# Performance work log

Measured on AMD Instinct MI355X. Metric: run time of the kernel, lower is better.

## Reference

```python
import jax, jax.numpy as jnp
import numpy as np

N = 1024      # n_nodes
F = 64        # n_features
L = 64        # lookback_window (must equal F for U1 @ B to typecheck, as in the torch code)
NDF = 4       # n_data_features
NTF = 8       # n_time_features
FC1 = 1024
FC2 = 512
K = 2         # kernel_size
DIL = (2, 2)  # dilation_list
DELTA = 0.05
EPS = 1e-5


def _ln(x, g, b):
    mu = x.mean(-1, keepdims=True)
    v = ((x - mu) ** 2).mean(-1, keepdims=True)
    return (x - mu) / jnp.sqrt(v + EPS) * g + b


def _mlp2(x, W1, b1, g, bb, W2, b2):
    h = jax.nn.relu(_ln(x @ W1 + b1, g, bb))
    return h @ W2 + b2


def setup_inputs() -> dict:
    ks = jax.random.split(jax.random.key(0), 16)
    def rn(i, shape, s=1.0):
        return jax.random.normal(ks[i], shape, dtype=jnp.float32) * s
    z = lambda *s: jnp.zeros(s, jnp.float32)
    o = lambda *s: jnp.ones(s, jnp.float32)
    return {
        "observation": rn(0, (N, NDF, L)),
        "time_features": rn(1, (L, NTF)),
        "layer_initial": rn(2, (L, N)),
        "sW1": rn(3, (N, 256), N ** -0.5), "sb1": z(256), "s_ln_g": o(256), "s_ln_b": z(256),
        "sW2": rn(4, (256, N * F), 256 ** -0.5), "sb2": z(N * F),
        "tW1": rn(5, (NTF, 256), NTF ** -0.5), "tb1": z(256), "t_ln_g": o(256), "t_ln_b": z(256),
        "tW2": rn(6, (256, N * F), 256 ** -0.5), "tb2": z(N * F),
        "B": o(F, F),
        "fW1": rn(7, (N * NDF, FC1), (N * NDF) ** -0.5), "fb1": z(FC1), "f1g": o(FC1), "f1b": z(FC1),
        "fW2": rn(8, (FC1, FC2), FC1 ** -0.5), "fb2": z(FC2), "f2g": o(FC2), "f2b": z(FC2),
        "fW3": rn(9, (FC2, N * F), FC2 ** -0.5), "fb3": z(N * F),
        "Wf": rn(10, (K, F, F)), "Wb": rn(11, (K, F, F)), "bconv": rn(12, (F,)),
    }


def _forward(observation, time_features, layer_initial, sW1, sb1, s_ln_g, s_ln_b, sW2, sb2,
             tW1, tb1, t_ln_g, t_ln_b, tW2, tb2, B,
             fW1, fb1, f1g, f1b, fW2, fb2, f2g, f2b, fW3, fb3, Wf, Wb, bconv):
    # GraphConstructor node embedding; U[:, :, j] is (N, L)
    emb = _mlp2(layer_initial, sW1, sb1, s_ln_g, s_ln_b, sW2, sb2) \
        + _mlp2(time_features, tW1, tb1, t_ln_g, t_ln_b, tW2, tb2)   # (L, N*F)
    U = emb.reshape(L, N, F).transpose(1, 0, 2)                      # (N, L, F)
    Uf = jnp.moveaxis(U, 2, 0)                                       # (F, N, L) for feature-axis gathers

    def adj(aidx, bidx):
        # batched adjacency: softmax over rows of thresholded U1 B U2^T, then D^-1/2 A D^-1/2
        Ua, Ub = Uf[aidx], Uf[bidx]                                  # (M, N, L)
        S = jax.lax.stop_gradient(jnp.einsum('mnl,lp,mqp->mnq', Ua, B, Ub))  # .detach() in torch
        S = jnp.where(S >= DELTA, S, 0.0)
        A = jax.nn.softmax(S, axis=-1)
        dn = 1.0 / jnp.sqrt(A.sum(-1))                               # degree is diagonal -> sqrtm/inverse = elementwise
        return A * dn[:, :, None] * dn[:, None, :]

    # fully_connected: observation (N, NDF, L) -> X (N, F, L)
    obs = observation.transpose(2, 0, 1).reshape(L, N * NDF)
    h = jax.nn.relu(_ln(obs @ fW1 + fb1, f1g, f1b))
    h = jax.nn.relu(_ln(h @ fW2 + fb2, f2g, f2b))
    X = (h @ fW3 + fb3).reshape(L, N, F).transpose(1, 2, 0)          # (N, F, L)

    gamma = 1
    outs = []
    for d in DIL:
        length = X.shape[-1]
        ts = np.arange(d - 1, length, d)                             # t with (t+1) % d == 0, static
        Z = jnp.zeros((ts.size, N, F), X.dtype)
        for k in range(K):
            tk = ts - k                                              # >= 0 since K <= min(DIL)
            Xk = X[:, :, tk]                                         # (N, F, M)
            A1 = adj((gamma * tk) % L, (gamma * ts) % L)             # pair (idx - k*gamma, idx)
            A2 = adj((gamma * ts) % L, (gamma * tk) % L)             # pair (idx, idx - k*gamma)
            msg = jnp.einsum('mnq,qfm->mnf', A1, Xk) @ Wf[k] \
                + jnp.einsum('mnq,qfm->mnf', A2, Xk) @ Wb[k] + bconv
            Z = Z + jnp.tanh(msg)
        X = jnp.moveaxis(Z, 0, 2)                                    # (N, F, M) becomes next layer input
        outs.append(X[:, :, -1])
        gamma *= d
    return jnp.stack(outs)                                           # (len(DIL), N, F)


def reference(observation, time_features, layer_initial, sW1, sb1, s_ln_g, s_ln_b, sW2, sb2,
              tW1, tb1, t_ln_g, t_ln_b, tW2, tb2, B,
              fW1, fb1, f1g, f1b, fW2, fb2, f2g, f2b, fW3, fb3, Wf, Wb, bconv):
    return _forward(observation, time_features, layer_initial, sW1, sb1, s_ln_g, s_ln_b, sW2, sb2,
                    tW1, tb1, t_ln_g, t_ln_b, tW2, tb2, B,
                    fW1, fb1, f1g, f1b, fW2, fb2, f2g, f2b, fW3, fb3, Wf, Wb, bconv)
```

## Files before the change

### kernel.cpp

```cpp
#include <hip/hip_runtime.h>
#include <cstddef>

#define EPS_C   1e-5f
#define DELTA_C 0.05f

struct Pairs { int a[6]; int b[6]; int t[6]; };


template<int K>
__device__ __forceinline__ void head_body(
    const float* __restrict__ A, const float* __restrict__ W1,
    const float* __restrict__ b1, const float* __restrict__ g,
    const float* __restrict__ bb, float* __restrict__ H,
    float* As, float* rs, float* rs2, int row, int j)
{
  for (int i = j; i < K; i += 256) As[i] = A[row * K + i];
  __syncthreads();

  float a0 = 0.f, a1 = 0.f, a2 = 0.f, a3 = 0.f;
  const float* __restrict__ Wp = W1 + j;
#pragma unroll 2
  for (int c = 0; c < K; c += 8) {
    float w0 = Wp[(size_t)(c + 0) * 256];
    float w1 = Wp[(size_t)(c + 1) * 256];
    float w2 = Wp[(size_t)(c + 2) * 256];
    float w3 = Wp[(size_t)(c + 3) * 256];
    float w4 = Wp[(size_t)(c + 4) * 256];
    float w5 = Wp[(size_t)(c + 5) * 256];
    float w6 = Wp[(size_t)(c + 6) * 256];
    float w7 = Wp[(size_t)(c + 7) * 256];
    a0 += As[c + 0] * w0 + As[c + 4] * w4;
    a1 += As[c + 1] * w1 + As[c + 5] * w5;
    a2 += As[c + 2] * w2 + As[c + 6] * w6;
    a3 += As[c + 3] * w3 + As[c + 7] * w7;
  }
  float acc = ((a0 + a1) + (a2 + a3)) + b1[j];

  rs[j] = acc; rs2[j] = acc * acc;
  __syncthreads();
  for (int st = 128; st > 0; st >>= 1) {
    if (j < st) { rs[j] += rs[j + st]; rs2[j] += rs2[j + st]; }
    __syncthreads();
  }
  float mu  = rs[0] * (1.f / 256.f);
  float var = rs2[0] * (1.f / 256.f) - mu * mu;
  float y = (acc - mu) * rsqrtf(var + EPS_C) * g[j] + bb[j];
  H[row * 256 + j] = fmaxf(y, 0.f);
}

template<int MODE>
__device__ __forceinline__ void skinny_body(
    const float* __restrict__ A, const float* __restrict__ W,
    float* __restrict__ part, int K, int N, int bid, int tid,
    float (*ARs)[64])
{
  int jblocks = N >> 8;
  int jb = bid % jblocks;
  int kc = bid / jblocks;
  int k0 = kc << 6;
  {
    int c = tid >> 6, i = tid & 63;
    int k = k0 + i;
    float v;
    if (MODE == 0) v = A[c * K + k];
    else { int n = k >> 2, df = k & 3; v = A[n * 256 + df * 64 + 60 + c]; }
    ARs[c][i] = v;
  }
  __syncthreads();
  int j = (jb << 8) + tid;
  float acc0 = 0.f, acc1 = 0.f, acc2 = 0.f, acc3 = 0.f;
#pragma unroll
  for (int kk = 0; kk < 64; kk += 16) {
    float w[16];
#pragma unroll
    for (int u = 0; u < 16; ++u) w[u] = W[(size_t)(k0 + kk + u) * N + j];
#pragma unroll
    for (int u = 0; u < 16; ++u) {
      acc0 += ARs[0][kk + u] * w[u];
      acc1 += ARs[1][kk + u] * w[u];
      acc2 += ARs[2][kk + u] * w[u];
      acc3 += ARs[3][kk + u] * w[u];
    }
  }
  part[(size_t)(kc * 4 + 0) * N + j] = acc0;
  part[(size_t)(kc * 4 + 1) * N + j] = acc1;
  part[(size_t)(kc * 4 + 2) * N + j] = acc2;
  part[(size_t)(kc * 4 + 3) * N + j] = acc3;
}

template<int N_, int PARTS>
__device__ __forceinline__ void red_body(
    const float* __restrict__ part, const float* __restrict__ bias,
    const float* __restrict__ g, const float* __restrict__ bb,
    float* __restrict__ out, int c, int tid, float* rs, float* rs2)
{
  constexpr int PER = N_ >> 8;
  float x[PER];
  float s = 0.f, s2 = 0.f;
#pragma unroll
  for (int i = 0; i < PER; ++i) {
    int j = (i << 8) + tid;
    float v = bias[j];
#pragma unroll 8
    for (int p = 0; p < PARTS; ++p) v += part[(size_t)(p * 4 + c) * N_ + j];
    x[i] = v; s += v; s2 += v * v;
  }
  rs[tid] = s; rs2[tid] = s2;
  __syncthreads();
  for (int st = 128; st > 0; st >>= 1) {
    if (tid < st) { rs[tid] += rs[tid + st]; rs2[tid] += rs2[tid + st]; }
    __syncthreads();
  }
  float mu  = rs[0] / (float)N_;
  float var = rs2[0] / (float)N_ - mu * mu;
  float inv = rsqrtf(var + EPS_C);
#pragma unroll
  for (int i = 0; i < PER; ++i) {
    int j = (i << 8) + tid;
    out[c * N_ + j] = fmaxf((x[i] - mu) * inv * g[j] + bb[j], 0.f);
  }
}


__global__ __launch_bounds__(256) void k1_heads_skinny(
    const float* __restrict__ layer_initial, const float* __restrict__ sW1,
    const float* __restrict__ sb1, const float* __restrict__ s_g,
    const float* __restrict__ s_b, float* __restrict__ Hs,
    const float* __restrict__ time_features, const float* __restrict__ tW1,
    const float* __restrict__ tb1, const float* __restrict__ t_g,
    const float* __restrict__ t_b, float* __restrict__ Ht,
    const float* __restrict__ observation, const float* __restrict__ fW1,
    float* __restrict__ part1)
{
  __shared__ float As[1024];
  __shared__ float rs[256], rs2[256];
  __shared__ float ARs[4][64];
  int bid = blockIdx.x, j = threadIdx.x;
  if (bid < 64) {
    head_body<1024>(layer_initial, sW1, sb1, s_g, s_b, Hs, As, rs, rs2, bid, j);
  } else if (bid < 128) {
    head_body<8>(time_features, tW1, tb1, t_g, t_b, Ht, As, rs, rs2, bid - 64, j);
  } else {
    skinny_body<1>(observation, fW1, part1, 4096, 1024, bid - 128, j, ARs);
  }
}

__global__ __launch_bounds__(256) void k2_emb_red1(
    const float* __restrict__ Hs, const float* __restrict__ Ht,
    const float* __restrict__ sW2, const float* __restrict__ sb2,
    const float* __restrict__ tW2, const float* __restrict__ tb2,
    float* __restrict__ Vs,
    const float* __restrict__ part1, const float* __restrict__ fb1,
    const float* __restrict__ f1g, const float* __restrict__ f1b,
    float* __restrict__ h1)
{
  __shared__ __align__(16) float HcT[64][68];
  __shared__ __align__(16) float Wc[64][20];
  int tid = threadIdx.x;
  if (blockIdx.x < 256) {
    int n0 = blockIdx.x * 4;
    int lq = tid >> 4, jc = tid & 15;
    int nn = n0 + (jc >> 2), cc = jc & 3;
    int kkw = tid >> 2, nloc = tid & 3;

    float4 hr[4]; float4 wr;
    {
      const float* __restrict__ Hsrc = Hs;
      const float* __restrict__ Wsrc = sW2;
#pragma unroll
      for (int i = 0; i < 4; ++i) {
        int flat = i * 1024 + tid * 4;
        int l = flat >> 6, kk = flat & 63;
        hr[i] = *(const float4*)&Hsrc[l * 256 + kk];
      }
      wr = *(const float4*)&Wsrc[(size_t)kkw * 65536 + (size_t)(n0 + nloc) * 64 + 60];
    }
    float acc0 = 0.f, acc1 = 0.f, acc2 = 0.f, acc3 = 0.f;
    for (int ch = 0; ch < 8; ++ch) {
      __syncthreads();
#pragma unroll
      for (int i = 0; i < 4; ++i) {
        int flat = i * 1024 + tid * 4;
        int l = flat >> 6, kk = flat & 63;
        HcT[kk + 0][l] = hr[i].x;
        HcT[kk + 1][l] = hr[i].y;
        HcT[kk + 2][l] = hr[i].z;
        HcT[kk + 3][l] = hr[i].w;
      }
      *(float4*)&Wc[kkw][nloc * 4] = wr;
      __syncthreads();
      if (ch < 7) {
        int nc2 = ch + 1;
        const float* __restrict__ Hsrc = (nc2 < 4) ? Hs : Ht;
        const float* __restrict__ Wsrc = (nc2 < 4) ? sW2 : tW2;
        int kl = (nc2 & 3) << 6;
#pragma unroll
        for (int i = 0; i < 4; ++i) {
          int flat = i * 1024 + tid * 4;
          int l = flat >> 6, kk = flat & 63;
          hr[i] = *(const float4*)&Hsrc[l * 256 + kl + kk];
        }
        wr = *(const float4*)&Wsrc[(size_t)(kl + kkw) * 65536 + (size_t)(n0 + nloc) * 64 + 60];
      }
#pragma unroll 8
      for (int kk = 0; kk < 64; ++kk) {
        float4 av = *(const float4*)&HcT[kk][lq * 4];
        float w = Wc[kk][jc];
        acc0 += av.x * w; acc1 += av.y * w; acc2 += av.z * w; acc3 += av.w * w;
      }
    }
    int jj = nn * 64 + 60 + cc;
    float bias = sb2[jj] + tb2[jj];
    float4 st = { acc0 + bias, acc1 + bias, acc2 + bias, acc3 + bias };
    *(float4*)&Vs[(size_t)cc * 65536 + (size_t)nn * 64 + lq * 4] = st;
  } else {
    red_body<1024, 64>(part1, fb1, f1g, f1b, h1, blockIdx.x - 256, tid,
                       &HcT[0][0], &HcT[0][0] + 256);
  }
}

__global__ __launch_bounds__(256) void k3_vab_skinny(
    const float* __restrict__ Vs, const float* __restrict__ Bmat,
    float* __restrict__ VaBt, float* __restrict__ VsT,
    const float* __restrict__ h1, const float* __restrict__ fW2,
    float* __restrict__ part2)
{
  __shared__ float Va[64][65], Bs[64][65];
  int tid = threadIdx.x;
  if (blockIdx.x < 64) {
    int c = blockIdx.x >> 4, nb = blockIdx.x & 15;
    int n0 = nb << 6;
    int rg = tid >> 4, cg = tid & 15;
#pragma unroll
    for (int i = 0; i < 4; ++i) {
      int flat = i * 1024 + tid * 4;
      int rr = flat >> 6, cc = flat & 63;
      float4 v = *(const float4*)&Vs[(size_t)c * 65536 + (size_t)(n0 + rr) * 64 + cc];
      Va[rr][cc] = v.x; Va[rr][cc+1] = v.y; Va[rr][cc+2] = v.z; Va[rr][cc+3] = v.w;
      float4 w = *(const float4*)&Bmat[flat];
      Bs[rr][cc] = w.x; Bs[rr][cc+1] = w.y; Bs[rr][cc+2] = w.z; Bs[rr][cc+3] = w.w;
    }
    __syncthreads();
#pragma unroll
    for (int i = 0; i < 4; ++i) {
      int flat = i * 1024 + tid * 4;
      int l = flat >> 6, nn = flat & 63;
      float4 st = { Va[nn][l], Va[nn+1][l], Va[nn+2][l], Va[nn+3][l] };
      *(float4*)&VsT[(size_t)c * 65536 + (size_t)l * 1024 + n0 + nn] = st;
    }
    float acc[4][4];
#pragma unroll
    for (int i = 0; i < 4; ++i)
#pragma unroll
      for (int j = 0; j < 4; ++j) acc[i][j] = 0.f;
#pragma unroll 4
    for (int l = 0; l < 64; ++l) {
      float av[4], bv[4];
#pragma unroll
      for (int i = 0; i < 4; ++i) av[i] = Va[rg * 4 + i][l];
#pragma unroll
      for (int j = 0; j < 4; ++j) bv[j] = Bs[l][cg * 4 + j];
#pragma unroll
      for (int i = 0; i < 4; ++i)
#pragma unroll
        for (int j = 0; j < 4; ++j) acc[i][j] += av[i] * bv[j];
    }
#pragma unroll
    for (int j = 0; j < 4; ++j) {
      float4 st = { acc[0][j], acc[1][j], acc[2][j], acc[3][j] };
      *(float4*)&VaBt[(size_t)c * 65536 + (size_t)(cg * 4 + j) * 1024 + n0 + rg * 4] = st;
    }
  } else {
    skinny_body<0>(h1, fW2, part2, 1024, 512, blockIdx.x - 64, tid,
                   (float(*)[64])&Va[0][0]);
  }
}

__global__ __launch_bounds__(256) void big_w3b(
    const float* __restrict__ part2, const float* __restrict__ fb2,
    const float* __restrict__ f2g, const float* __restrict__ f2b,
    const float* __restrict__ fW3, const float* __restrict__ fb3,
    float* __restrict__ Xr)
{
  int tid = threadIdx.x;
  __shared__ float h2s[2048];
  __shared__ float sm[4][128];
  {
    int c = tid >> 6, lane = tid & 63;
    float v[8]; float s = 0.f, s2 = 0.f;
#pragma unroll
    for (int k = 0; k < 8; ++k) {
      int j = lane + k * 64;
      float x = fb2[j];
#pragma unroll
      for (int p = 0; p < 16; ++p) x += part2[(size_t)(p * 4 + c) * 512 + j];
      v[k] = x; s += x; s2 += x * x;
    }
#pragma unroll
    for (int off = 1; off < 64; off <<= 1) {
      s += __shfl_xor(s, off); s2 += __shfl_xor(s2, off);
    }
    float mu = s * (1.f / 512.f);
    float var = s2 * (1.f / 512.f) - mu * mu;
    float inv = rsqrtf(var + EPS_C);
#pragma unroll
    for (int k = 0; k < 8; ++k) {
      int j = lane + k * 64;
      h2s[c * 512 + j] = fmaxf((v[k] - mu) * inv * f2g[j] + f2b[j], 0.f);
    }
  }
  __syncthreads();

  int col = tid & 127, ks = tid >> 7;
  int j = blockIdx.x * 128 + col;
  int kbase = ks << 8;
  float acc0 = 0.f, acc1 = 0.f, acc2 = 0.f, acc3 = 0.f;
  for (int k0 = 0; k0 < 256; k0 += 16) {
    float w[16];
#pragma unroll
    for (int u = 0; u < 16; ++u) w[u] = fW3[(size_t)(kbase + k0 + u) * 65536 + j];
#pragma unroll
    for (int u = 0; u < 16; ++u) {
      int k = kbase + k0 + u;
      acc0 += h2s[k]        * w[u];
      acc1 += h2s[512 + k]  * w[u];
      acc2 += h2s[1024 + k] * w[u];
      acc3 += h2s[1536 + k] * w[u];
    }
  }
  if (ks) { sm[0][col] = acc0; sm[1][col] = acc1; sm[2][col] = acc2; sm[3][col] = acc3; }
  __syncthreads();
  if (!ks) {
    float b = fb3[j];
    Xr[j]            = acc0 + sm[0][col] + b;
    Xr[65536 + j]    = acc1 + sm[1][col] + b;
    Xr[131072 + j]   = acc2 + sm[2][col] + b;
    Xr[196608 + j]   = acc3 + sm[3][col] + b;
  }
}

template<int NSPLIT>
__global__ __launch_bounds__(256) void attn_partial(
    const float* __restrict__ VaBt, const float* __restrict__ VsT,
    const float* __restrict__ Xbase, float* __restrict__ Pl,
    float* __restrict__ ml, Pairs pr)
{
  constexpr int TILES = 16 / NSPLIT;
  int pi  = blockIdx.x / (16 * NSPLIT);
  int rem = blockIdx.x % (16 * NSPLIT);
  int nb  = rem / NSPLIT;
  int s   = rem % NSPLIT;
  int n0  = nb << 6;
  int tid = threadIdx.x;
  int rg = tid >> 4, cg = tid & 15;
  int rg4 = rg * 4, cg4 = cg * 4;
  int a = pr.a[pi], b = pr.b[pi], t = pr.t[pi];

  __shared__ __align__(16) float VaT[64][68];
  __shared__ __align__(16) float VbT[64][68];
  __shared__ __align__(16) float Xs[64][68];
  float (*St)[68] = VbT;

#pragma unroll
  for (int i = 0; i < 4; ++i) {
    int flat = i * 1024 + tid * 4;
    int p = flat >> 6, nn = flat & 63;
    float4 v = *(const float4*)&VaBt[(size_t)a * 65536 + (size_t)p * 1024 + n0 + nn];
    *(float4*)&VaT[p][nn] = v;
  }
  float m_run[4], l_run[4];
#pragma unroll
  for (int i = 0; i < 4; ++i) { m_run[i] = -1e30f; l_run[i] = 0.f; }
  float P[4][4];
#pragma unroll
  for (int i = 0; i < 4; ++i)
#pragma unroll
    for (int j = 0; j < 4; ++j) P[i][j] = 0.f;
  __syncthreads();

  for (int ti = 0; ti < TILES; ++ti) {
    int q0 = (s * TILES + ti) << 6;
    if (ti) __syncthreads();
#pragma unroll
    for (int i = 0; i < 4; ++i) {
      int flat = i * 1024 + tid * 4;
      int p = flat >> 6, qq = flat & 63;
      float4 v = *(const float4*)&VsT[(size_t)b * 65536 + (size_t)p * 1024 + q0 + qq];
      *(float4*)&VbT[p][qq] = v;
      float4 x = *(const float4*)&Xbase[(size_t)t * 65536 + (size_t)(q0 + p) * 64 + qq];
      *(float4*)&Xs[p][qq] = x;
    }
    __syncthreads();
    float sa[4][4];
#pragma unroll
    for (int i = 0; i < 4; ++i)
#pragma unroll
      for (int j = 0; j < 4; ++j) sa[i][j] = 0.f;
#pragma unroll 4
    for (int p = 0; p < 64; ++p) {
      float av[4], bv[4];
      *(float4*)av = *(const float4*)&VaT[p][rg4];
      *(float4*)bv = *(const float4*)&VbT[p][cg4];
#pragma unroll
      for (int i = 0; i < 4; ++i)
#pragma unroll
        for (int j = 0; j < 4; ++j) sa[i][j] += av[i] * bv[j];
    }
    float scv[4];
#pragma unroll
    for (int i = 0; i < 4; ++i) {
#pragma unroll
      for (int j = 0; j < 4; ++j) sa[i][j] = (sa[i][j] >= DELTA_C) ? sa[i][j] : 0.f;
      float tm = fmaxf(fmaxf(sa[i][0], sa[i][1]), fmaxf(sa[i][2], sa[i][3]));
      tm = fmaxf(tm, __shfl_xor(tm, 1));
      tm = fmaxf(tm, __shfl_xor(tm, 2));
      tm = fmaxf(tm, __shfl_xor(tm, 4));
      tm = fmaxf(tm, __shfl_xor(tm, 8));
      float mnew = fmaxf(m_run[i], tm);
      float sc = __expf(m_run[i] - mnew);
      float ssum = 0.f;
#pragma unroll
      for (int j = 0; j < 4; ++j) {
        float e = __expf(sa[i][j] - mnew);
        sa[i][j] = e;
        ssum += e;
      }
      ssum += __shfl_xor(ssum, 1);
      ssum += __shfl_xor(ssum, 2);
      ssum += __shfl_xor(ssum, 4);
      ssum += __shfl_xor(ssum, 8);
      l_run[i] = l_run[i] * sc + ssum;
      m_run[i] = mnew;
      scv[i] = sc;
    }
    __syncthreads();
#pragma unroll
    for (int i = 0; i < 4; ++i) {
      float4 e4 = { sa[i][0], sa[i][1], sa[i][2], sa[i][3] };
      *(float4*)&St[rg4 + i][cg4] = e4;
    }
    __syncthreads();
#pragma unroll
    for (int i = 0; i < 4; ++i)
#pragma unroll
      for (int j = 0; j < 4; ++j) P[i][j] *= scv[i];
#pragma unroll 2
    for (int q4 = 0; q4 < 64; q4 += 4) {
      float4 ev[4], xv[4];
#pragma unroll
      for (int i = 0; i < 4; ++i) ev[i] = *(const float4*)&St[rg4 + i][q4];
#pragma unroll
      for (int u = 0; u < 4; ++u) xv[u] = *(const float4*)&Xs[q4 + u][cg4];
#pragma unroll
      for (int i = 0; i < 4; ++i) {
        const float* e = &ev[i].x;
#pragma unroll
        for (int u = 0; u < 4; ++u) {
          const float* x = &xv[u].x;
#pragma unroll
          for (int j = 0; j < 4; ++j) P[i][j] += e[u] * x[j];
        }
      }
    }
  }
  size_t base = (size_t)((pi * 16 + nb) * NSPLIT + s);
  float* pp = Pl + base * 4096;
#pragma unroll
  for (int i = 0; i < 4; ++i) {
    float4 st = { P[i][0], P[i][1], P[i][2], P[i][3] };
    *(float4*)&pp[(size_t)(rg4 + i) * 64 + cg4] = st;
  }
  if ((tid & 15) == 0) {
    float* mlp = ml + base * 128;
#pragma unroll
    for (int i = 0; i < 4; ++i) {
      mlp[rg4 + i]      = m_run[i];
      mlp[64 + rg4 + i] = l_run[i];
    }
  }
}

template<int NS_T>
__global__ __launch_bounds__(256) void merge_partial(
    const float* __restrict__ Pl, const float* __restrict__ ml,
    const float* __restrict__ Wf, const float* __restrict__ Wb,
    float* __restrict__ Gp)
{
  int mm = blockIdx.x / 48;
  int rem = blockIdx.x % 48;
  int nb = rem / 3, inst = rem % 3;
  int n0 = nb << 6;
  int tid = threadIdx.x;
  int rg = tid >> 4, cg = tid & 15;
  int rg4 = rg * 4, cg4 = cg * 4;
  int r = tid >> 2, sub = tid & 3;

  __shared__ __align__(16) float PtT[64][68];
  __shared__ __align__(16) float Wt[64][68];

  size_t base = (size_t)((mm * 3 + inst) * 16 + nb) * NS_T;
  const float* mlp = ml + base * 128;
  float mg = -1e30f;
#pragma unroll
  for (int s2 = 0; s2 < NS_T; ++s2) mg = fmaxf(mg, mlp[s2 * 128 + r]);
  float acc[16];
#pragma unroll
  for (int u = 0; u < 16; ++u) acc[u] = 0.f;
  float lg = 0.f;
#pragma unroll
  for (int s2 = 0; s2 < NS_T; ++s2) {
    float f = __expf(mlp[s2 * 128 + r] - mg);
    lg += f * mlp[s2 * 128 + 64 + r];
    const float4* ps = (const float4*)(Pl + (base + s2) * 4096 + r * 64 + sub * 16);
#pragma unroll
    for (int u = 0; u < 4; ++u) {
      float4 v = ps[u];
      acc[u*4+0] += f * v.x; acc[u*4+1] += f * v.y;
      acc[u*4+2] += f * v.z; acc[u*4+3] += f * v.w;
    }
  }
  float inv = 1.f / lg;
#pragma unroll
  for (int u = 0; u < 16; ++u) PtT[sub * 16 + u][r] = acc[u] * inv;
  for (int i = tid; i < 4096; i += 256) {
    int rr = i >> 6, cc = i & 63;
    float w;
    if (inst == 0)      w = Wf[i] + Wb[i];
    else if (inst == 1) w = Wf[4096 + i];
    else                w = Wb[4096 + i];
    Wt[rr][cc] = w;
  }
  __syncthreads();
  float g2[4][4];
#pragma unroll
  for (int i = 0; i < 4; ++i)
#pragma unroll
    for (int j = 0; j < 4; ++j) g2[i][j] = 0.f;
#pragma unroll 4
  for (int ff = 0; ff < 64; ++ff) {
    float p[4], w[4];
    *(float4*)p = *(const float4*)&PtT[ff][rg4];
    *(float4*)w = *(const float4*)&Wt[ff][cg4];
#pragma unroll
    for (int i = 0; i < 4; ++i)
#pragma unroll
      for (int j = 0; j < 4; ++j) g2[i][j] += p[i] * w[j];
  }
#pragma unroll
  for (int i = 0; i < 4; ++i) {
    float4 st = { g2[i][0], g2[i][1], g2[i][2], g2[i][3] };
    *(float4*)&Gp[(size_t)(mm * 3 + inst) * 65536 + (size_t)(n0 + rg4 + i) * 64 + cg4] = st;
  }
}

__global__ __launch_bounds__(256) void finalize_z(
    const float* __restrict__ Gp, const float* __restrict__ bconv,
    float* __restrict__ dst0, float* __restrict__ dst1, float* __restrict__ extra1)
{
  int mm = blockIdx.x >> 4;
  int nb = blockIdx.x & 15;
  int tid = threadIdx.x;
  size_t tileOff = (size_t)(nb << 6) * 64;
  const float* g0 = Gp + (size_t)(mm * 3 + 0) * 65536 + tileOff;
  const float* g1 = Gp + (size_t)(mm * 3 + 1) * 65536 + tileOff;
  const float* g2 = Gp + (size_t)(mm * 3 + 2) * 65536 + tileOff;
  float* dst = (mm == 0) ? dst0 : dst1;
  for (int i = tid * 4; i < 4096; i += 1024) {
    float4 a = *(const float4*)&g0[i];
    float4 b = *(const float4*)&g1[i];
    float4 c = *(const float4*)&g2[i];
    int col = i & 63;
    float4 z;
    z.x = tanhf(a.x + bconv[col+0]) + tanhf(b.x + c.x + bconv[col+0]);
    z.y = tanhf(a.y + bconv[col+1]) + tanhf(b.y + c.y + bconv[col+1]);
    z.z = tanhf(a.z + bconv[col+2]) + tanhf(b.z + c.z + bconv[col+2]);
    z.w = tanhf(a.w + bconv[col+3]) + tanhf(b.w + c.w + bconv[col+3]);
    *(float4*)&dst[tileOff + i] = z;
    if (mm == 1 && extra1) *(float4*)&extra1[tileOff + i] = z;
  }
}

extern "C" void kernel_launch(void* const* d_in, const int* in_sizes, int n_in,
                              void* d_out, int out_size, void* d_ws, size_t ws_size,
                              hipStream_t stream)
{
  const float* observation   = (const float*)d_in[0];
  const float* time_features = (const float*)d_in[1];
  const float* layer_initial = (const float*)d_in[2];
  const float* sW1   = (const float*)d_in[3];
  const float* sb1   = (const float*)d_in[4];
  const float* s_ln_g = (const float*)d_in[5];
  const float* s_ln_b = (const float*)d_in[6];
  const float* sW2   = (const float*)d_in[7];
  const float* sb2   = (const float*)d_in[8];
  const float* tW1   = (const float*)d_in[9];
  const float* tb1   = (const float*)d_in[10];
  const float* t_ln_g = (const float*)d_in[11];
  const float* t_ln_b = (const float*)d_in[12];
  const float* tW2   = (const float*)d_in[13];
  const float* tb2   = (const float*)d_in[14];
  const float* Bmat  = (const float*)d_in[15];
  const float* fW1   = (const float*)d_in[16];
  const float* fb1   = (const float*)d_in[17];
  const float* f1g   = (const float*)d_in[18];
  const float* f1b   = (const float*)d_in[19];
  const float* fW2   = (const float*)d_in[20];
  const float* fb2   = (const float*)d_in[21];
  const float* f2g   = (const float*)d_in[22];
  const float* f2b   = (const float*)d_in[23];
  const float* fW3   = (const float*)d_in[24];
  const float* fb3   = (const float*)d_in[25];
  const float* Wf    = (const float*)d_in[26];
  const float* Wb    = (const float*)d_in[27];
  const float* bconv = (const float*)d_in[28];
  float* out = (float*)d_out;

  float* ws    = (float*)d_ws;
  float* Hs    = ws;
  float* Ht    = Hs    + 16384;
  float* Vs    = Ht    + 16384;
  float* VsT   = Vs    + 262144;
  float* VaBt  = VsT   + 262144;
  float* part1 = VaBt  + 262144;
  float* part2 = part1 + 262144;
  float* h1    = part2 + 32768;
  float* Xr    = h1    + 4096;
  float* Pl    = Xr    + 262144;
  float* ml    = Pl    + 3145728;
  float* Pl2   = ml    + 98304;
  float* ml2   = Pl2   + 3145728;
  float* Z1    = ml2   + 98304;
  float* Gp    = Z1    + 131072;

  k1_heads_skinny<<<384, 256, 0, stream>>>(
      layer_initial, sW1, sb1, s_ln_g, s_ln_b, Hs,
      time_features, tW1, tb1, t_ln_g, t_ln_b, Ht,
      observation, fW1, part1);
  k2_emb_red1<<<260, 256, 0, stream>>>(
      Hs, Ht, sW2, sb2, tW2, tb2, Vs,
      part1, fb1, f1g, f1b, h1);
  k3_vab_skinny<<<96, 256, 0, stream>>>(Vs, Bmat, VaBt, VsT, h1, fW2, part2);
  big_w3b<<<512, 256, 0, stream>>>(part2, fb2, f2g, f2b, fW3, fb3, Xr);

  Pairs pA;
  pA.a[0]=1; pA.b[0]=1; pA.t[0]=1;
  pA.a[1]=0; pA.b[1]=1; pA.t[1]=0;
  pA.a[2]=1; pA.b[2]=0; pA.t[2]=0;
  pA.a[3]=3; pA.b[3]=3; pA.t[3]=3;
  pA.a[4]=2; pA.b[4]=3; pA.t[4]=2;
  pA.a[5]=3; pA.b[5]=2; pA.t[5]=2;
  attn_partial<8><<<6 * 16 * 8, 256, 0, stream>>>(VaBt, VsT, Xr, Pl, ml, pA);
  merge_partial<8><<<96, 256, 0, stream>>>(Pl, ml, Wf, Wb, Gp);
  finalize_z<<<32, 256, 0, stream>>>(Gp, bconv, Z1, Z1 + 65536, out);

  Pairs pB;
  pB.a[0]=2; pB.b[0]=2; pB.t[0]=1;
  pB.a[1]=0; pB.b[1]=2; pB.t[1]=0;
  pB.a[2]=2; pB.b[2]=0; pB.t[2]=0;
  pB.a[3]=pB.a[4]=pB.a[5]=0; pB.b[3]=pB.b[4]=pB.b[5]=0; pB.t[3]=pB.t[4]=pB.t[5]=0;
  attn_partial<16><<<3 * 16 * 16, 256, 0, stream>>>(VaBt, VsT, Z1, Pl2, ml2, pB);
  merge_partial<16><<<48, 256, 0, stream>>>(Pl2, ml2, Wf, Wb, Gp);
  finalize_z<<<16, 256, 0, stream>>>(Gp, bconv, out + 65536, nullptr, nullptr);
}
```

Before: 164.0 us.

## Split-K the sW1 head, rebalance stage fusion, and widen merge grid

The 1024-wide sW1 head GEMV is split across four K-chunks per row, giving 256 blocks instead of 64. A new small kernel reduces the partials and applies LayerNorm, and it also absorbs the fc1 reduction. The kernel pipeline is re-paired: the embedding GEMM is fused with the fW2 skinny stage, and the fc2 reduction with the VaB stage, so big_w3c only loads a precomputed h2. merge_partial now uses 16-row tiles with four times as many blocks to raise parallelism. In exchange it adds one kernel launch and extra global round trips for Hp and h2.

Measured after the change: 151.2 us, median of 3. 1.08x faster.

```diff
diff --git a/kernel.cpp b/kernel.cpp
--- a/kernel.cpp
+++ b/kernel.cpp
@@ -17,24 +17,11 @@
   for (int i = j; i < K; i += 256) As[i] = A[row * K + i];
   __syncthreads();
 
-  float a0 = 0.f, a1 = 0.f, a2 = 0.f, a3 = 0.f;
+  float a0 = 0.f;
   const float* __restrict__ Wp = W1 + j;
-#pragma unroll 2
-  for (int c = 0; c < K; c += 8) {
-    float w0 = Wp[(size_t)(c + 0) * 256];
-    float w1 = Wp[(size_t)(c + 1) * 256];
-    float w2 = Wp[(size_t)(c + 2) * 256];
-    float w3 = Wp[(size_t)(c + 3) * 256];
-    float w4 = Wp[(size_t)(c + 4) * 256];
-    float w5 = Wp[(size_t)(c + 5) * 256];
-    float w6 = Wp[(size_t)(c + 6) * 256];
-    float w7 = Wp[(size_t)(c + 7) * 256];
-    a0 += As[c + 0] * w0 + As[c + 4] * w4;
-    a1 += As[c + 1] * w1 + As[c + 5] * w5;
-    a2 += As[c + 2] * w2 + As[c + 6] * w6;
-    a3 += As[c + 3] * w3 + As[c + 7] * w7;
-  }
-  float acc = ((a0 + a1) + (a2 + a3)) + b1[j];
+#pragma unroll
+  for (int c = 0; c < K; ++c) a0 += As[c] * Wp[(size_t)c * 256];
+  float acc = a0 + b1[j];
 
   rs[j] = acc; rs2[j] = acc * acc;
   __syncthreads();
@@ -124,35 +111,85 @@
 
 __global__ __launch_bounds__(256) void k1_heads_skinny(
     const float* __restrict__ layer_initial, const float* __restrict__ sW1,
-    const float* __restrict__ sb1, const float* __restrict__ s_g,
-    const float* __restrict__ s_b, float* __restrict__ Hs,
+    float* __restrict__ Hp,
     const float* __restrict__ time_features, const float* __restrict__ tW1,
     const float* __restrict__ tb1, const float* __restrict__ t_g,
     const float* __restrict__ t_b, float* __restrict__ Ht,
     const float* __restrict__ observation, const float* __restrict__ fW1,
     float* __restrict__ part1)
 {
-  __shared__ float As[1024];
+  __shared__ float As[256];
   __shared__ float rs[256], rs2[256];
   __shared__ float ARs[4][64];
   int bid = blockIdx.x, j = threadIdx.x;
-  if (bid < 64) {
-    head_body<1024>(layer_initial, sW1, sb1, s_g, s_b, Hs, As, rs, rs2, bid, j);
-  } else if (bid < 128) {
-    head_body<8>(time_features, tW1, tb1, t_g, t_b, Ht, As, rs, rs2, bid - 64, j);
+  if (bid < 256) {
+    int kc = bid >> 6, row = bid & 63;
+    int k0 = kc << 8;
+    As[j] = layer_initial[row * 1024 + k0 + j];
+    __syncthreads();
+    float a0 = 0.f, a1 = 0.f, a2 = 0.f, a3 = 0.f;
+    const float* __restrict__ Wp = sW1 + (size_t)k0 * 256 + j;
+#pragma unroll 2
+    for (int c = 0; c < 256; c += 8) {
+      float w0 = Wp[(size_t)(c + 0) * 256];
+      float w1 = Wp[(size_t)(c + 1) * 256];
+      float w2 = Wp[(size_t)(c + 2) * 256];
+      float w3 = Wp[(size_t)(c + 3) * 256];
+      float w4 = Wp[(size_t)(c + 4) * 256];
+      float w5 = Wp[(size_t)(c + 5) * 256];
+      float w6 = Wp[(size_t)(c + 6) * 256];
+      float w7 = Wp[(size_t)(c + 7) * 256];
+      a0 += As[c + 0] * w0 + As[c + 4] * w4;
+      a1 += As[c + 1] * w1 + As[c + 5] * w5;
+      a2 += As[c + 2] * w2 + As[c + 6] * w6;
+      a3 += As[c + 3] * w3 + As[c + 7] * w7;
+    }
+    Hp[(size_t)(kc * 64 + row) * 256 + j] = (a0 + a1) + (a2 + a3);
+  } else if (bid < 320) {
+    head_body<8>(time_features, tW1, tb1, t_g, t_b, Ht, As, rs, rs2, bid - 256, j);
   } else {
-    skinny_body<1>(observation, fW1, part1, 4096, 1024, bid - 128, j, ARs);
-  }
-}
-
-__global__ __launch_bounds__(256) void k2_emb_red1(
+    skinny_body<1>(observation, fW1, part1, 4096, 1024, bid - 320, j, ARs);
+  }
+}
+
+__global__ __launch_bounds__(256) void k2_headred_red1(
+    const float* __restrict__ Hp, const float* __restrict__ sb1,
+    const float* __restrict__ s_g, const float* __restrict__ s_b,
+    float* __restrict__ Hs,
+    const float* __restrict__ part1, const float* __restrict__ fb1,
+    const float* __restrict__ f1g, const float* __restrict__ f1b,
+    float* __restrict__ h1)
+{
+  __shared__ float rs[256], rs2[256];
+  int tid = threadIdx.x;
+  if (blockIdx.x < 64) {
+    int row = blockIdx.x;
+    float acc = sb1[tid];
+#pragma unroll
+    for (int kc = 0; kc < 4; ++kc)
+      acc += Hp[(size_t)(kc * 64 + row) * 256 + tid];
+    rs[tid] = acc; rs2[tid] = acc * acc;
+    __syncthreads();
+    for (int st = 128; st > 0; st >>= 1) {
+      if (tid < st) { rs[tid] += rs[tid + st]; rs2[tid] += rs2[tid + st]; }
+      __syncthreads();
+    }
+    float mu  = rs[0] * (1.f / 256.f);
+    float var = rs2[0] * (1.f / 256.f) - mu * mu;
+    float y = (acc - mu) * rsqrtf(var + EPS_C) * s_g[tid] + s_b[tid];
+    Hs[row * 256 + tid] = fmaxf(y, 0.f);
+  } else {
+    red_body<1024, 64>(part1, fb1, f1g, f1b, h1, blockIdx.x - 64, tid, rs, rs2);
+  }
+}
+
+__global__ __launch_bounds__(256) void k3_emb_skinny(
     const float* __restrict__ Hs, const float* __restrict__ Ht,
     const float* __restrict__ sW2, const float* __restrict__ sb2,
     const float* __restrict__ tW2, const float* __restrict__ tb2,
     float* __restrict__ Vs,
-    const float* __restrict__ part1, const float* __restrict__ fb1,
-    const float* __restrict__ f1g, const float* __restrict__ f1b,
-    float* __restrict__ h1)
+    const float* __restrict__ h1, const float* __restrict__ fW2,
+    float* __restrict__ part2)
 {
   __shared__ __align__(16) float HcT[64][68];
   __shared__ __align__(16) float Wc[64][20];
@@ -165,15 +202,13 @@
 
     float4 hr[4]; float4 wr;
     {
-      const float* __restrict__ Hsrc = Hs;
-      const float* __restrict__ Wsrc = sW2;
 #pragma unroll
       for (int i = 0; i < 4; ++i) {
         int flat = i * 1024 + tid * 4;
         int l = flat >> 6, kk = flat & 63;
-        hr[i] = *(const float4*)&Hsrc[l * 256 + kk];
+        hr[i] = *(const float4*)&Hs[l * 256 + kk];
       }
-      wr = *(const float4*)&Wsrc[(size_t)kkw * 65536 + (size_t)(n0 + nloc) * 64 + 60];
+      wr = *(const float4*)&sW2[(size_t)kkw * 65536 + (size_t)(n0 + nloc) * 64 + 60];
     }
     float acc0 = 0.f, acc1 = 0.f, acc2 = 0.f, acc3 = 0.f;
     for (int ch = 0; ch < 8; ++ch) {
@@ -214,21 +249,26 @@
     float4 st = { acc0 + bias, acc1 + bias, acc2 + bias, acc3 + bias };
     *(float4*)&Vs[(size_t)cc * 65536 + (size_t)nn * 64 + lq * 4] = st;
   } else {
-    red_body<1024, 64>(part1, fb1, f1g, f1b, h1, blockIdx.x - 256, tid,
-                       &HcT[0][0], &HcT[0][0] + 256);
-  }
-}
-
-__global__ __launch_bounds__(256) void k3_vab_skinny(
+    skinny_body<0>(h1, fW2, part2, 1024, 512, blockIdx.x - 256, tid,
+                   (float(*)[64])&HcT[0][0]);
+  }
+}
+
+__global__ __launch_bounds__(256) void k4_red2_vab(
+    const float* __restrict__ part2, const float* __restrict__ fb2,
+    const float* __restrict__ f2g, const float* __restrict__ f2b,
+    float* __restrict__ h2,
     const float* __restrict__ Vs, const float* __restrict__ Bmat,
-    float* __restrict__ VaBt, float* __restrict__ VsT,
-    const float* __restrict__ h1, const float* __restrict__ fW2,
-    float* __restrict__ part2)
+    float* __restrict__ VaBt, float* __restrict__ VsT)
 {
   __shared__ float Va[64][65], Bs[64][65];
   int tid = threadIdx.x;
-  if (blockIdx.x < 64) {
-    int c = blockIdx.x >> 4, nb = blockIdx.x & 15;
+  if (blockIdx.x < 4) {
+    red_body<512, 16>(part2, fb2, f2g, f2b, h2, blockIdx.x, tid,
+                      &Va[0][0], &Bs[0][0]);
+  } else {
+    int bid = blockIdx.x - 4;
+    int c = bid >> 4, nb = bid & 15;
     int n0 = nb << 6;
     int rg = tid >> 4, cg = tid & 15;
 #pragma unroll
@@ -270,50 +310,21 @@
       float4 st = { acc[0][j], acc[1][j], acc[2][j], acc[3][j] };
       *(float4*)&VaBt[(size_t)c * 65536 + (size_t)(cg * 4 + j) * 1024 + n0 + rg * 4] = st;
     }
-  } else {
-    skinny_body<0>(h1, fW2, part2, 1024, 512, blockIdx.x - 64, tid,
-                   (float(*)[64])&Va[0][0]);
-  }
-}
-
-__global__ __launch_bounds__(256) void big_w3b(
-    const float* __restrict__ part2, const float* __restrict__ fb2,
-    const float* __restrict__ f2g, const float* __restrict__ f2b,
-    const float* __restrict__ fW3, const float* __restrict__ fb3,
-    float* __restrict__ Xr)
+  }
+}
+
+__global__ __launch_bounds__(256) void big_w3c(
+    const float* __restrict__ h2, const float* __restrict__ fW3,
+    const float* __restrict__ fb3, float* __restrict__ Xr)
 {
   int tid = threadIdx.x;
   __shared__ float h2s[2048];
   __shared__ float sm[4][128];
-  {
-    int c = tid >> 6, lane = tid & 63;
-    float v[8]; float s = 0.f, s2 = 0.f;
-#pragma unroll
-    for (int k = 0; k < 8; ++k) {
-      int j = lane + k * 64;
-      float x = fb2[j];
-#pragma unroll
-      for (int p = 0; p < 16; ++p) x += part2[(size_t)(p * 4 + c) * 512 + j];
-      v[k] = x; s += x; s2 += x * x;
-    }
-#pragma unroll
-    for (int off = 1; off < 64; off <<= 1) {
-      s += __shfl_xor(s, off); s2 += __shfl_xor(s2, off);
-    }
-    float mu = s * (1.f / 512.f);
-    float var = s2 * (1.f / 512.f) - mu * mu;
-    float inv = rsqrtf(var + EPS_C);
-#pragma unroll
-    for (int k = 0; k < 8; ++k) {
-      int j = lane + k * 64;
-      h2s[c * 512 + j] = fmaxf((v[k] - mu) * inv * f2g[j] + f2b[j], 0.f);
-    }
-  }
-  __syncthreads();
-
+  for (int i = tid; i < 2048; i += 256) h2s[i] = h2[i];
   int col = tid & 127, ks = tid >> 7;
   int j = blockIdx.x * 128 + col;
   int kbase = ks << 8;
+  __syncthreads();
   float acc0 = 0.f, acc1 = 0.f, acc2 = 0.f, acc3 = 0.f;
   for (int k0 = 0; k0 < 256; k0 += 16) {
     float w[16];
@@ -481,47 +492,40 @@
 }
 
 template<int NS_T>
-__global__ __launch_bounds__(256) void merge_partial(
+__global__ __launch_bounds__(256) void merge_partial16(
     const float* __restrict__ Pl, const float* __restrict__ ml,
     const float* __restrict__ Wf, const float* __restrict__ Wb,
     float* __restrict__ Gp)
 {
-  int mm = blockIdx.x / 48;
-  int rem = blockIdx.x % 48;
-  int nb = rem / 3, inst = rem % 3;
-  int n0 = nb << 6;
+  int mm  = blockIdx.x / 192;
+  int rem = blockIdx.x % 192;
+  int nb  = rem / 12;
+  int r2  = rem % 12;
+  int nq  = r2 / 3, inst = r2 % 3;
   int tid = threadIdx.x;
-  int rg = tid >> 4, cg = tid & 15;
-  int rg4 = rg * 4, cg4 = cg * 4;
-  int r = tid >> 2, sub = tid & 3;
-
-  __shared__ __align__(16) float PtT[64][68];
+  int r = tid >> 4, fq = tid & 15;
+
+  __shared__ __align__(16) float Ps[16][68];
   __shared__ __align__(16) float Wt[64][68];
 
   size_t base = (size_t)((mm * 3 + inst) * 16 + nb) * NS_T;
   const float* mlp = ml + base * 128;
+  int rowi = nq * 16 + r;
   float mg = -1e30f;
 #pragma unroll
-  for (int s2 = 0; s2 < NS_T; ++s2) mg = fmaxf(mg, mlp[s2 * 128 + r]);
-  float acc[16];
-#pragma unroll
-  for (int u = 0; u < 16; ++u) acc[u] = 0.f;
+  for (int s2 = 0; s2 < NS_T; ++s2) mg = fmaxf(mg, mlp[s2 * 128 + rowi]);
+  float acc[4] = {0.f, 0.f, 0.f, 0.f};
   float lg = 0.f;
 #pragma unroll
   for (int s2 = 0; s2 < NS_T; ++s2) {
-    float f = __expf(mlp[s2 * 128 + r] - mg);
-    lg += f * mlp[s2 * 128 + 64 + r];
-    const float4* ps = (const float4*)(Pl + (base + s2) * 4096 + r * 64 + sub * 16);
-#pragma unroll
-    for (int u = 0; u < 4; ++u) {
-      float4 v = ps[u];
-      acc[u*4+0] += f * v.x; acc[u*4+1] += f * v.y;
-      acc[u*4+2] += f * v.z; acc[u*4+3] += f * v.w;
-    }
+    float f = __expf(mlp[s2 * 128 + rowi] - mg);
+    lg += f * mlp[s2 * 128 + 64 + rowi];
+    float4 v = *(const float4*)(Pl + (base + s2) * 4096 + rowi * 64 + fq * 4);
+    acc[0] += f * v.x; acc[1] += f * v.y; acc[2] += f * v.z; acc[3] += f * v.w;
   }
   float inv = 1.f / lg;
-#pragma unroll
-  for (int u = 0; u < 16; ++u) PtT[sub * 16 + u][r] = acc[u] * inv;
+  float4 pv = { acc[0] * inv, acc[1] * inv, acc[2] * inv, acc[3] * inv };
+  *(float4*)&Ps[r][fq * 4] = pv;
   for (int i = tid; i < 4096; i += 256) {
     int rr = i >> 6, cc = i & 63;
     float w;
@@ -531,26 +535,16 @@
     Wt[rr][cc] = w;
   }
   __syncthreads();
-  float g2[4][4];
-#pragma unroll
-  for (int i = 0; i < 4; ++i)
-#pragma unroll
-    for (int j = 0; j < 4; ++j) g2[i][j] = 0.f;
-#pragma unroll 4
-  for (int ff = 0; ff < 64; ++ff) {
-    float p[4], w[4];
-    *(float4*)p = *(const float4*)&PtT[ff][rg4];
-    *(float4*)w = *(const float4*)&Wt[ff][cg4];
-#pragma unroll
-    for (int i = 0; i < 4; ++i)
-#pragma unroll
-      for (int j = 0; j < 4; ++j) g2[i][j] += p[i] * w[j];
-  }
-#pragma unroll
-  for (int i = 0; i < 4; ++i) {
-    float4 st = { g2[i][0], g2[i][1], g2[i][2], g2[i][3] };
-    *(float4*)&Gp[(size_t)(mm * 3 + inst) * 65536 + (size_t)(n0 + rg4 + i) * 64 + cg4] = st;
-  }
+  float g0 = 0.f, g1 = 0.f, g2 = 0.f, g3 = 0.f;
+#pragma unroll 8
+  for (int f = 0; f < 64; ++f) {
+    float p = Ps[r][f];
+    float4 w4 = *(const float4*)&Wt[f][fq * 4];
+    g0 += p * w4.x; g1 += p * w4.y; g2 += p * w4.z; g3 += p * w4.w;
+  }
+  float4 st = { g0, g1, g2, g3 };
+  *(float4*)&Gp[(size_t)(mm * 3 + inst) * 65536 +
+                (size_t)(nb * 64 + nq * 16 + r) * 64 + fq * 4] = st;
 }
 
 __global__ __launch_bounds__(256) void finalize_z(
@@ -618,13 +612,15 @@
   float* ws    = (float*)d_ws;
   float* Hs    = ws;
   float* Ht    = Hs    + 16384;
-  float* Vs    = Ht    + 16384;
+  float* Hp    = Ht    + 16384;
+  float* Vs    = Hp    + 65536;
   float* VsT   = Vs    + 262144;
   float* VaBt  = VsT   + 262144;
   float* part1 = VaBt  + 262144;
   float* part2 = part1 + 262144;
   float* h1    = part2 + 32768;
-  float* Xr    = h1    + 4096;
+  float* h2    = h1    + 4096;
+  float* Xr    = h2    + 2048;
   float* Pl    = Xr    + 262144;
   float* ml    = Pl    + 3145728;
   float* Pl2   = ml    + 98304;
@@ -632,15 +628,18 @@
   float* Z1    = ml2   + 98304;
   float* Gp    = Z1    + 131072;
 
-  k1_heads_skinny<<<384, 256, 0, stream>>>(
-      layer_initial, sW1, sb1, s_ln_g, s_ln_b, Hs,
+  k1_heads_skinny<<<576, 256, 0, stream>>>(
+      layer_initial, sW1, Hp,
       time_features, tW1, tb1, t_ln_g, t_ln_b, Ht,
       observation, fW1, part1);
-  k2_emb_red1<<<260, 256, 0, stream>>>(
-      Hs, Ht, sW2, sb2, tW2, tb2, Vs,
+  k2_headred_red1<<<68, 256, 0, stream>>>(
+      Hp, sb1, s_ln_g, s_ln_b, Hs,
       part1, fb1, f1g, f1b, h1);
-  k3_vab_skinny<<<96, 256, 0, stream>>>(Vs, Bmat, VaBt, VsT, h1, fW2, part2);
-  big_w3b<<<512, 256, 0, stream>>>(part2, fb2, f2g, f2b, fW3, fb3, Xr);
+  k3_emb_skinny<<<288, 256, 0, stream>>>(
+      Hs, Ht, sW2, sb2, tW2, tb2, Vs, h1, fW2, part2);
+  k4_red2_vab<<<68, 256, 0, stream>>>(
+      part2, fb2, f2g, f2b, h2, Vs, Bmat, VaBt, VsT);
+  big_w3c<<<512, 256, 0, stream>>>(h2, fW3, fb3, Xr);
 
   Pairs pA;
   pA.a[0]=1; pA.b[0]=1; pA.t[0]=1;
@@ -650,7 +649,7 @@
   pA.a[4]=2; pA.b[4]=3; pA.t[4]=2;
   pA.a[5]=3; pA.b[5]=2; pA.t[5]=2;
   attn_partial<8><<<6 * 16 * 8, 256, 0, stream>>>(VaBt, VsT, Xr, Pl, ml, pA);
-  merge_partial<8><<<96, 256, 0, stream>>>(Pl, ml, Wf, Wb, Gp);
+  merge_partial16<8><<<384, 256, 0, stream>>>(Pl, ml, Wf, Wb, Gp);
   finalize_z<<<32, 256, 0, stream>>>(Gp, bconv, Z1, Z1 + 65536, out);
 
   Pairs pB;
@@ -659,6 +658,6 @@
   pB.a[2]=2; pB.b[2]=0; pB.t[2]=0;
   pB.a[3]=pB.a[4]=pB.a[5]=0; pB.b[3]=pB.b[4]=pB.b[5]=0; pB.t[3]=pB.t[4]=pB.t[5]=0;
   attn_partial<16><<<3 * 16 * 16, 256, 0, stream>>>(VaBt, VsT, Z1, Pl2, ml2, pB);
-  merge_partial<16><<<48, 256, 0, stream>>>(Pl2, ml2, Wf, Wb, Gp);
+  merge_partial16<16><<<192, 256, 0, stream>>>(Pl2, ml2, Wf, Wb, Gp);
   finalize_z<<<16, 256, 0, stream>>>(Gp, bconv, out + 65536, nullptr, nullptr);
 }
```
